# Kernel tuning notes

Measured on AMD Instinct MI355X. Metric: run time of the kernel, lower is better.

Reference implementation:

```python
import jax, jax.numpy as jnp
import numpy as np
import math

B, L, H, E = 4, 2048, 16, 64
S, D = L, E


def setup_inputs() -> dict:
    key = jax.random.key(0)
    kq, kk, kv = jax.random.split(key, 3)
    queries = jax.random.normal(kq, (B, L, H, E), dtype=jnp.float32)
    keys = jax.random.normal(kk, (B, S, H, E), dtype=jnp.float32)
    values = jax.random.normal(kv, (B, S, H, D), dtype=jnp.float32)
    # TriangularCausalMask: True above the diagonal => masked out
    attn_mask = jnp.broadcast_to(
        jnp.triu(jnp.ones((L, S), dtype=bool), k=1)[None, None], (B, 1, L, S)
    )
    return {"queries": queries, "keys": keys, "values": values, "attn_mask": attn_mask}


def reference(queries, keys, values, attn_mask):
    Edim = queries.shape[-1]
    scale = 1.0 / math.sqrt(Edim)  # self.scale is None -> 1/sqrt(E)
    # scores: [B, H, L, S]
    scores = jnp.einsum("blhe,bshe->bhls", queries, keys)
    # mask BEFORE scaling (as in original); -inf is invariant under positive scale
    scores = jnp.where(attn_mask, -jnp.inf, scores)
    attn = jax.nn.softmax(scale * scores, axis=-1)  # dropout p=0.0 -> identity
    out = jnp.einsum("bhls,bshd->blhd", attn, values)
    return out
```

## Files before the change

kernel.cpp:

```cpp
#include <hip/hip_runtime.h>


#define B_ 4
#define L_ 2048
#define H_ 16

typedef __attribute__((ext_vector_type(4))) float f32x4;
typedef __attribute__((ext_vector_type(8))) short bf16x8;

__device__ __forceinline__ unsigned pkbf(float lo, float hi) {
    union { float f; unsigned u; } a, b;
    a.f = lo; b.f = hi;
    return __builtin_amdgcn_perm(b.u, a.u, 0x07060302u);
}

__global__ __launch_bounds__(256, 2) void attn_fwd(
    const float* __restrict__ Q, const float* __restrict__ K,
    const float* __restrict__ V, float* __restrict__ O)
{
    __shared__ unsigned smem[8704];
    unsigned* Kl = smem;
    unsigned* Vl = smem + 2304;
    unsigned* Pl = smem + 4608;

    const int tid = threadIdx.x;
    const int w   = tid >> 6;
    const int l   = tid & 63;
    const int l15 = l & 15;
    const int qd  = l >> 4;
    const int bh  = blockIdx.x & 63;
    const int pr  = blockIdx.x >> 6;
    const int b   = bh >> 4, h = bh & 15;
    const float cexp = 0.125f * 1.44269504088896340736f;

    const float* Kb = K + (((size_t)b * L_) * H_ + h) * 64;
    const float* Vb = V + (((size_t)b * L_) * H_ + h) * 64;
    unsigned* Pw = Pl + w * 1024;

    const int krow = tid >> 2, kq = tid & 3;
    const int vsp  = tid >> 3, vdg = tid & 7;
    const int vswz = vsp ^ (4 * vdg);

    for (int ph = 0; ph < 2; ++ph) {
        const int t    = ph ? pr : 15 - pr;
        const int qr0  = t * 128 + w * 32;
        const int mykb = (qr0 >> 6) + 1;
        const int nkb  = 2 * (t + 1);

        bf16x8 qf[2][2];
#pragma unroll
        for (int rt = 0; rt < 2; ++rt) {
            const int row = qr0 + 16 * rt + l15;
            const float* qp = Q + (((size_t)b * L_ + row) * H_ + h) * 64 + qd * 8;
#pragma unroll
            for (int ke = 0; ke < 2; ++ke) {
                float4 f0 = *(const float4*)(qp + ke * 32);
                float4 f1 = *(const float4*)(qp + ke * 32 + 4);
                union { unsigned u[4]; bf16x8 v; } cv;
                cv.u[0] = pkbf(f0.x * cexp, f0.y * cexp);
                cv.u[1] = pkbf(f0.z * cexp, f0.w * cexp);
                cv.u[2] = pkbf(f1.x * cexp, f1.y * cexp);
                cv.u[3] = pkbf(f1.z * cexp, f1.w * cexp);
                qf[rt][ke] = cv.v;
            }
        }

        f32x4 o[4][2];
#pragma unroll
        for (int dt = 0; dt < 4; ++dt)
#pragma unroll
            for (int rt = 0; rt < 2; ++rt)
                o[dt][rt] = (f32x4){0.f, 0.f, 0.f, 0.f};
        float ls[2] = {0.f, 0.f};

        for (int kb = 0; kb < nkb; ++kb) {
            __syncthreads();
            {
                const float* kg = Kb + (size_t)(kb * 64 + krow) * 1024 + kq * 16;
                float4 a0 = *(const float4*)(kg + 0);
                float4 a1 = *(const float4*)(kg + 4);
                float4 a2 = *(const float4*)(kg + 8);
                float4 a3 = *(const float4*)(kg + 12);
                unsigned* kd = Kl + krow * 36 + kq * 8;
                uint4 w0, w1;
                w0.x = pkbf(a0.x, a0.y); w0.y = pkbf(a0.z, a0.w);
                w0.z = pkbf(a1.x, a1.y); w0.w = pkbf(a1.z, a1.w);
                w1.x = pkbf(a2.x, a2.y); w1.y = pkbf(a2.z, a2.w);
                w1.z = pkbf(a3.x, a3.y); w1.w = pkbf(a3.z, a3.w);
                *(uint4*)kd = w0;
                *(uint4*)(kd + 4) = w1;
            }
            {
                const float* vg = Vb + (size_t)(kb * 64 + 2 * vsp) * 1024 + vdg * 8;
                float4 b0 = *(const float4*)(vg + 0);
                float4 b1 = *(const float4*)(vg + 4);
                float4 c0 = *(const float4*)(vg + 1024);
                float4 c1 = *(const float4*)(vg + 1028);
                unsigned* vd = Vl + (8 * vdg) * 36 + vswz;
                vd[0 * 36] = pkbf(b0.x, c0.x);
                vd[1 * 36] = pkbf(b0.y, c0.y);
                vd[2 * 36] = pkbf(b0.z, c0.z);
                vd[3 * 36] = pkbf(b0.w, c0.w);
                vd[4 * 36] = pkbf(b1.x, c1.x);
                vd[5 * 36] = pkbf(b1.y, c1.y);
                vd[6 * 36] = pkbf(b1.z, c1.z);
                vd[7 * 36] = pkbf(b1.w, c1.w);
            }
            __syncthreads();
            if (kb >= mykb) continue;

            f32x4 st[4][2];
#pragma unroll
            for (int kt = 0; kt < 4; ++kt)
#pragma unroll
                for (int rt = 0; rt < 2; ++rt)
                    st[kt][rt] = (f32x4){0.f, 0.f, 0.f, 0.f};
#pragma unroll
            for (int kt = 0; kt < 4; ++kt)
#pragma unroll
                for (int ke = 0; ke < 2; ++ke) {
                    bf16x8 a = *(const bf16x8*)(Kl + (kt * 16 + l15) * 36 + ke * 16 + qd * 4);
                    st[kt][0] = __builtin_amdgcn_mfma_f32_16x16x32_bf16(a, qf[0][ke], st[kt][0], 0, 0, 0);
                    st[kt][1] = __builtin_amdgcn_mfma_f32_16x16x32_bf16(a, qf[1][ke], st[kt][1], 0, 0, 0);
                }

            if (kb == mykb - 1) {
#pragma unroll
                for (int kt = 0; kt < 4; ++kt)
#pragma unroll
                    for (int rt = 0; rt < 2; ++rt) {
                        const int rowg = qr0 + 16 * rt + l15;
#pragma unroll
                        for (int r = 0; r < 4; ++r) {
                            const int key = kb * 64 + kt * 16 + 4 * qd + r;
                            if (key > rowg) st[kt][rt][r] = -1e30f;
                        }
                    }
            }

            float sacc0 = 0.f, sacc1 = 0.f;
#pragma unroll
            for (int kt = 0; kt < 4; ++kt)
#pragma unroll
                for (int r = 0; r < 4; ++r) {
                    float p0 = exp2f(st[kt][0][r]);
                    float p1 = exp2f(st[kt][1][r]);
                    st[kt][0][r] = p0;
                    st[kt][1][r] = p1;
                    sacc0 += p0;
                    sacc1 += p1;
                }
            ls[0] += sacc0;
            ls[1] += sacc1;

#pragma unroll
            for (int kt = 0; kt < 4; ++kt)
#pragma unroll
                for (int rt = 0; rt < 2; ++rt) {
                    uint2 pv;
                    pv.x = pkbf(st[kt][rt][0], st[kt][rt][1]);
                    pv.y = pkbf(st[kt][rt][2], st[kt][rt][3]);
                    const int reader = 32 * (kt & 1) + 16 * (qd >> 1) + l15;
                    *(uint2*)(Pw + (kt >> 1) * 512 + rt * 256 + reader * 4 + 2 * (qd & 1)) = pv;
                }

            bf16x8 vf[2][4];
#pragma unroll
            for (int se = 0; se < 2; ++se)
#pragma unroll
                for (int dt = 0; dt < 4; ++dt) {
                    const int col = (se * 16 + qd * 4) ^ (4 * (2 * dt + (l15 >> 3)));
                    vf[se][dt] = *(const bf16x8*)(Vl + (dt * 16 + l15) * 36 + col);
                }

#pragma unroll
            for (int se = 0; se < 2; ++se)
#pragma unroll
                for (int rt = 0; rt < 2; ++rt) {
                    bf16x8 pb = *(const bf16x8*)(Pw + se * 512 + rt * 256 + l * 4);
#pragma unroll
                    for (int dt = 0; dt < 4; ++dt)
                        o[dt][rt] = __builtin_amdgcn_mfma_f32_16x16x32_bf16(vf[se][dt], pb, o[dt][rt], 0, 0, 0);
                }
        }

#pragma unroll
        for (int rt = 0; rt < 2; ++rt) {
            float s = ls[rt];
            s += __shfl_xor(s, 16);
            s += __shfl_xor(s, 32);
            const float inv = 1.0f / s;
            const int row = qr0 + 16 * rt + l15;
            float* op = O + (((size_t)b * L_ + row) * H_ + h) * 64 + qd * 4;
#pragma unroll
            for (int dt = 0; dt < 4; ++dt) {
                float4 wv;
                wv.x = o[dt][rt][0] * inv;
                wv.y = o[dt][rt][1] * inv;
                wv.z = o[dt][rt][2] * inv;
                wv.w = o[dt][rt][3] * inv;
                *(float4*)(op + dt * 16) = wv;
            }
        }
    }
}

extern "C" void kernel_launch(void* const* d_in, const int* in_sizes, int n_in,
                              void* d_out, int out_size, void* d_ws, size_t ws_size,
                              hipStream_t stream) {
    const float* Q = (const float*)d_in[0];
    const float* K = (const float*)d_in[1];
    const float* V = (const float*)d_in[2];
    float* O = (float*)d_out;

    dim3 grid(64 * 8);
    dim3 block(256);
    hipLaunchKernelGGL(attn_fwd, grid, block, 0, stream, Q, K, V, O);
}
```

Baseline: 238.8 us.

## Double-buffer K/V tiles in LDS with register prefetch of next block

Splits the K/V LDS staging into two buffers and loads the next key block from global memory into registers before computing on the current block, then writes it to the alternate buffer. The aim is to hide global load latency behind the MFMA/softmax work and cut one barrier per iteration. It also swizzles the P scratch layout to avoid LDS bank conflicts and uses the raw hardware exp2 builtin. The cost is more LDS per block (about 52KB), which may limit occupancy, plus higher register pressure from the prefetched values.

```diff
diff --git a/kernel.cpp b/kernel.cpp
--- a/kernel.cpp
+++ b/kernel.cpp
@@ -7,6 +7,18 @@
 
 typedef __attribute__((ext_vector_type(4))) float f32x4;
 typedef __attribute__((ext_vector_type(8))) short bf16x8;
+
+#if __has_builtin(__builtin_amdgcn_exp2f)
+#define EXP2(x) __builtin_amdgcn_exp2f(x)
+#else
+#define EXP2(x) exp2f(x)
+#endif
+
+#if __has_builtin(__builtin_amdgcn_sched_barrier)
+#define SCHED_FENCE() __builtin_amdgcn_sched_barrier(0)
+#else
+#define SCHED_FENCE()
+#endif
 
 __device__ __forceinline__ unsigned pkbf(float lo, float hi) {
     union { float f; unsigned u; } a, b;
@@ -18,10 +30,8 @@
     const float* __restrict__ Q, const float* __restrict__ K,
     const float* __restrict__ V, float* __restrict__ O)
 {
-    __shared__ unsigned smem[8704];
-    unsigned* Kl = smem;
-    unsigned* Vl = smem + 2304;
-    unsigned* Pl = smem + 4608;
+    __shared__ unsigned smem[13312];
+    unsigned* Pl = smem + 9216;
 
     const int tid = threadIdx.x;
     const int w   = tid >> 6;
@@ -40,6 +50,7 @@
     const int krow = tid >> 2, kq = tid & 3;
     const int vsp  = tid >> 3, vdg = tid & 7;
     const int vswz = vsp ^ (4 * vdg);
+    const int grpr = l ^ (4 * ((l >> 4) & 1));
 
     for (int ph = 0; ph < 2; ++ph) {
         const int t    = ph ? pr : 15 - pr;
@@ -73,115 +84,154 @@
                 o[dt][rt] = (f32x4){0.f, 0.f, 0.f, 0.f};
         float ls[2] = {0.f, 0.f};
 
+        {
+            const float* kg = Kb + (size_t)krow * 1024 + kq * 16;
+            float4 k0 = *(const float4*)(kg + 0);
+            float4 k1 = *(const float4*)(kg + 4);
+            float4 k2 = *(const float4*)(kg + 8);
+            float4 k3 = *(const float4*)(kg + 12);
+            const float* vg = Vb + (size_t)(2 * vsp) * 1024 + vdg * 8;
+            float4 v0 = *(const float4*)(vg + 0);
+            float4 v1 = *(const float4*)(vg + 4);
+            float4 v2 = *(const float4*)(vg + 1024);
+            float4 v3 = *(const float4*)(vg + 1028);
+            unsigned* kd = smem + krow * 36 + kq * 8;
+            uint4 w0, w1;
+            w0.x = pkbf(k0.x, k0.y); w0.y = pkbf(k0.z, k0.w);
+            w0.z = pkbf(k1.x, k1.y); w0.w = pkbf(k1.z, k1.w);
+            w1.x = pkbf(k2.x, k2.y); w1.y = pkbf(k2.z, k2.w);
+            w1.z = pkbf(k3.x, k3.y); w1.w = pkbf(k3.z, k3.w);
+            *(uint4*)kd = w0;
+            *(uint4*)(kd + 4) = w1;
+            unsigned* vd = smem + 2304 + (8 * vdg) * 36 + vswz;
+            vd[0 * 36] = pkbf(v0.x, v2.x);
+            vd[1 * 36] = pkbf(v0.y, v2.y);
+            vd[2 * 36] = pkbf(v0.z, v2.z);
+            vd[3 * 36] = pkbf(v0.w, v2.w);
+            vd[4 * 36] = pkbf(v1.x, v3.x);
+            vd[5 * 36] = pkbf(v1.y, v3.y);
+            vd[6 * 36] = pkbf(v1.z, v3.z);
+            vd[7 * 36] = pkbf(v1.w, v3.w);
+        }
+        __syncthreads();
+
         for (int kb = 0; kb < nkb; ++kb) {
-            __syncthreads();
-            {
-                const float* kg = Kb + (size_t)(kb * 64 + krow) * 1024 + kq * 16;
-                float4 a0 = *(const float4*)(kg + 0);
-                float4 a1 = *(const float4*)(kg + 4);
-                float4 a2 = *(const float4*)(kg + 8);
-                float4 a3 = *(const float4*)(kg + 12);
-                unsigned* kd = Kl + krow * 36 + kq * 8;
+            const bool more = (kb + 1 < nkb);
+            float4 nk0, nk1, nk2, nk3, nv0, nv1, nv2, nv3;
+            if (more) {
+                const float* kg = Kb + (size_t)((kb + 1) * 64 + krow) * 1024 + kq * 16;
+                nk0 = *(const float4*)(kg + 0);
+                nk1 = *(const float4*)(kg + 4);
+                nk2 = *(const float4*)(kg + 8);
+                nk3 = *(const float4*)(kg + 12);
+                const float* vg = Vb + (size_t)((kb + 1) * 64 + 2 * vsp) * 1024 + vdg * 8;
+                nv0 = *(const float4*)(vg + 0);
+                nv1 = *(const float4*)(vg + 4);
+                nv2 = *(const float4*)(vg + 1024);
+                nv3 = *(const float4*)(vg + 1028);
+            }
+
+            if (kb < mykb) {
+                const unsigned* Kl = smem + (kb & 1) * 4608;
+                const unsigned* Vl = Kl + 2304;
+
+                f32x4 st[4][2];
+#pragma unroll
+                for (int kt = 0; kt < 4; ++kt)
+#pragma unroll
+                    for (int rt = 0; rt < 2; ++rt)
+                        st[kt][rt] = (f32x4){0.f, 0.f, 0.f, 0.f};
+#pragma unroll
+                for (int kt = 0; kt < 4; ++kt)
+#pragma unroll
+                    for (int ke = 0; ke < 2; ++ke) {
+                        bf16x8 a = *(const bf16x8*)(Kl + (kt * 16 + l15) * 36 + ke * 16 + qd * 4);
+                        st[kt][0] = __builtin_amdgcn_mfma_f32_16x16x32_bf16(a, qf[0][ke], st[kt][0], 0, 0, 0);
+                        st[kt][1] = __builtin_amdgcn_mfma_f32_16x16x32_bf16(a, qf[1][ke], st[kt][1], 0, 0, 0);
+                    }
+
+                if (kb == mykb - 1) {
+#pragma unroll
+                    for (int kt = 0; kt < 4; ++kt)
+#pragma unroll
+                        for (int rt = 0; rt < 2; ++rt) {
+                            const int rowg = qr0 + 16 * rt + l15;
+#pragma unroll
+                            for (int r = 0; r < 4; ++r) {
+                                const int key = kb * 64 + kt * 16 + 4 * qd + r;
+                                if (key > rowg) st[kt][rt][r] = -1e30f;
+                            }
+                        }
+                }
+
+                float sacc0 = 0.f, sacc1 = 0.f;
+#pragma unroll
+                for (int kt = 0; kt < 4; ++kt)
+#pragma unroll
+                    for (int r = 0; r < 4; ++r) {
+                        float p0 = EXP2(st[kt][0][r]);
+                        float p1 = EXP2(st[kt][1][r]);
+                        st[kt][0][r] = p0;
+                        st[kt][1][r] = p1;
+                        sacc0 += p0;
+                        sacc1 += p1;
+                    }
+                ls[0] += sacc0;
+                ls[1] += sacc1;
+
+#pragma unroll
+                for (int kt = 0; kt < 4; ++kt)
+#pragma unroll
+                    for (int rt = 0; rt < 2; ++rt) {
+                        uint2 pv;
+                        pv.x = pkbf(st[kt][rt][0], st[kt][rt][1]);
+                        pv.y = pkbf(st[kt][rt][2], st[kt][rt][3]);
+                        const int grp = (32 * (kt & 1) + 16 * (qd >> 1) + l15) ^ (4 * (qd >> 1));
+                        *(uint2*)(Pw + (kt >> 1) * 512 + rt * 256 + grp * 4 + 2 * (qd & 1)) = pv;
+                    }
+
+                bf16x8 vf[2][4];
+#pragma unroll
+                for (int se = 0; se < 2; ++se)
+#pragma unroll
+                    for (int dt = 0; dt < 4; ++dt) {
+                        const int col = (se * 16 + qd * 4) ^ (4 * (2 * dt + (l15 >> 3)));
+                        vf[se][dt] = *(const bf16x8*)(Vl + (dt * 16 + l15) * 36 + col);
+                    }
+
+#pragma unroll
+                for (int se = 0; se < 2; ++se)
+#pragma unroll
+                    for (int rt = 0; rt < 2; ++rt) {
+                        bf16x8 pb = *(const bf16x8*)(Pw + se * 512 + rt * 256 + grpr * 4);
+#pragma unroll
+                        for (int dt = 0; dt < 4; ++dt)
+                            o[dt][rt] = __builtin_amdgcn_mfma_f32_16x16x32_bf16(vf[se][dt], pb, o[dt][rt], 0, 0, 0);
+                    }
+            }
+
+            if (more) {
+                SCHED_FENCE();
+                unsigned* bK = smem + ((kb + 1) & 1) * 4608;
+                unsigned* kd = bK + krow * 36 + kq * 8;
                 uint4 w0, w1;
-                w0.x = pkbf(a0.x, a0.y); w0.y = pkbf(a0.z, a0.w);
-                w0.z = pkbf(a1.x, a1.y); w0.w = pkbf(a1.z, a1.w);
-                w1.x = pkbf(a2.x, a2.y); w1.y = pkbf(a2.z, a2.w);
-                w1.z = pkbf(a3.x, a3.y); w1.w = pkbf(a3.z, a3.w);
+                w0.x = pkbf(nk0.x, nk0.y); w0.y = pkbf(nk0.z, nk0.w);
+                w0.z = pkbf(nk1.x, nk1.y); w0.w = pkbf(nk1.z, nk1.w);
+                w1.x = pkbf(nk2.x, nk2.y); w1.y = pkbf(nk2.z, nk2.w);
+                w1.z = pkbf(nk3.x, nk3.y); w1.w = pkbf(nk3.z, nk3.w);
                 *(uint4*)kd = w0;
                 *(uint4*)(kd + 4) = w1;
-            }
-            {
-                const float* vg = Vb + (size_t)(kb * 64 + 2 * vsp) * 1024 + vdg * 8;
-                float4 b0 = *(const float4*)(vg + 0);
-                float4 b1 = *(const float4*)(vg + 4);
-                float4 c0 = *(const float4*)(vg + 1024);
-                float4 c1 = *(const float4*)(vg + 1028);
-                unsigned* vd = Vl + (8 * vdg) * 36 + vswz;
-                vd[0 * 36] = pkbf(b0.x, c0.x);
-                vd[1 * 36] = pkbf(b0.y, c0.y);
-                vd[2 * 36] = pkbf(b0.z, c0.z);
-                vd[3 * 36] = pkbf(b0.w, c0.w);
-                vd[4 * 36] = pkbf(b1.x, c1.x);
-                vd[5 * 36] = pkbf(b1.y, c1.y);
-                vd[6 * 36] = pkbf(b1.z, c1.z);
-                vd[7 * 36] = pkbf(b1.w, c1.w);
-            }
-            __syncthreads();
-            if (kb >= mykb) continue;
-
-            f32x4 st[4][2];
-#pragma unroll
-            for (int kt = 0; kt < 4; ++kt)
-#pragma unroll
-                for (int rt = 0; rt < 2; ++rt)
-                    st[kt][rt] = (f32x4){0.f, 0.f, 0.f, 0.f};
-#pragma unroll
-            for (int kt = 0; kt < 4; ++kt)
-#pragma unroll
-                for (int ke = 0; ke < 2; ++ke) {
-                    bf16x8 a = *(const bf16x8*)(Kl + (kt * 16 + l15) * 36 + ke * 16 + qd * 4);
-                    st[kt][0] = __builtin_amdgcn_mfma_f32_16x16x32_bf16(a, qf[0][ke], st[kt][0], 0, 0, 0);
-                    st[kt][1] = __builtin_amdgcn_mfma_f32_16x16x32_bf16(a, qf[1][ke], st[kt][1], 0, 0, 0);
-                }
-
-            if (kb == mykb - 1) {
-#pragma unroll
-                for (int kt = 0; kt < 4; ++kt)
-#pragma unroll
-                    for (int rt = 0; rt < 2; ++rt) {
-                        const int rowg = qr0 + 16 * rt + l15;
-#pragma unroll
-                        for (int r = 0; r < 4; ++r) {
-                            const int key = kb * 64 + kt * 16 + 4 * qd + r;
-                            if (key > rowg) st[kt][rt][r] = -1e30f;
-                        }
-                    }
-            }
-
-            float sacc0 = 0.f, sacc1 = 0.f;
-#pragma unroll
-            for (int kt = 0; kt < 4; ++kt)
-#pragma unroll
-                for (int r = 0; r < 4; ++r) {
-                    float p0 = exp2f(st[kt][0][r]);
-                    float p1 = exp2f(st[kt][1][r]);
-                    st[kt][0][r] = p0;
-                    st[kt][1][r] = p1;
-                    sacc0 += p0;
-                    sacc1 += p1;
-                }
-            ls[0] += sacc0;
-            ls[1] += sacc1;
-
-#pragma unroll
-            for (int kt = 0; kt < 4; ++kt)
-#pragma unroll
-                for (int rt = 0; rt < 2; ++rt) {
-                    uint2 pv;
-                    pv.x = pkbf(st[kt][rt][0], st[kt][rt][1]);
-                    pv.y = pkbf(st[kt][rt][2], st[kt][rt][3]);
-                    const int reader = 32 * (kt & 1) + 16 * (qd >> 1) + l15;
-                    *(uint2*)(Pw + (kt >> 1) * 512 + rt * 256 + reader * 4 + 2 * (qd & 1)) = pv;
-                }
-
-            bf16x8 vf[2][4];
-#pragma unroll
-            for (int se = 0; se < 2; ++se)
-#pragma unroll
-                for (int dt = 0; dt < 4; ++dt) {
-                    const int col = (se * 16 + qd * 4) ^ (4 * (2 * dt + (l15 >> 3)));
-                    vf[se][dt] = *(const bf16x8*)(Vl + (dt * 16 + l15) * 36 + col);
-                }
-
-#pragma unroll
-            for (int se = 0; se < 2; ++se)
-#pragma unroll
-                for (int rt = 0; rt < 2; ++rt) {
-                    bf16x8 pb = *(const bf16x8*)(Pw + se * 512 + rt * 256 + l * 4);
-#pragma unroll
-                    for (int dt = 0; dt < 4; ++dt)
-                        o[dt][rt] = __builtin_amdgcn_mfma_f32_16x16x32_bf16(vf[se][dt], pb, o[dt][rt], 0, 0, 0);
-                }
+                unsigned* vd = bK + 2304 + (8 * vdg) * 36 + vswz;
+                vd[0 * 36] = pkbf(nv0.x, nv2.x);
+                vd[1 * 36] = pkbf(nv0.y, nv2.y);
+                vd[2 * 36] = pkbf(nv0.z, nv2.z);
+                vd[3 * 36] = pkbf(nv0.w, nv2.w);
+                vd[4 * 36] = pkbf(nv1.x, nv3.x);
+                vd[5 * 36] = pkbf(nv1.y, nv3.y);
+                vd[6 * 36] = pkbf(nv1.z, nv3.z);
+                vd[7 * 36] = pkbf(nv1.w, nv3.w);
+                __syncthreads();
+            }
         }
 
 #pragma unroll
@@ -202,6 +252,7 @@
                 *(float4*)(op + dt * 16) = wv;
             }
         }
+        if (ph == 0) __syncthreads();
     }
 }
 
```

Result: faster. 210.2 us (-12.0%).
